# Optimization experiments

Measured on AMD Instinct MI355X. Metric: run time of the kernel, lower is better.

Reference implementation:

```python
import jax, jax.numpy as jnp
import numpy as np

BAND = 8          # band_width
DS = 0.1          # diag_subtract
DILATIONS = (1, 2, 4)
EPS_NORM = 1e-6
EPS_GAP = 1e-6
EPS_LN = 1e-5


def _conv1d(x, w, b, dil=1):
    # x: (B, C_in, T), w: (C_out, C_in, K) torch-style OIH
    pad = dil * (w.shape[-1] // 2)  # 'same' padding as in torch module
    y = jax.lax.conv_general_dilated(
        x, w, window_strides=(1,), padding=[(pad, pad)],
        rhs_dilation=(dil,), dimension_numbers=("NCH", "OIH", "NCH"))
    return y + b[None, :, None]


def _strip(feat, mask, w, ds):
    # Banded cosine SSM: strip[b, idx, t] = ((xn[b,t].xn[b,t+|k|]) - ds*[k==0] + 1)/2 * m[t]*m[t+|k|]
    # Mathematically identical to full S = xn xn^T (symmetric) followed by
    # extract_diagonal_strip, but computes only the (2w+1)-wide band.
    xm = feat * mask[:, :, None]
    xn = xm / (jnp.linalg.norm(xm, axis=-1, keepdims=True) + EPS_NORM)
    T = xn.shape[1]
    rows = []
    for k in range(-w, w + 1):
        a = abs(k)
        dot = jnp.einsum("btd,btd->bt", xn[:, :T - a] if a else xn, xn[:, a:])
        s = (dot - (ds if k == 0 else 0.0) + 1.0) * 0.5
        s = s * mask[:, :T - a] * mask[:, a:] if a else s * mask * mask
        rows.append(jnp.pad(s, ((0, 0), (0, a))))
    return jnp.stack(rows, axis=1)  # (B, 2w+1, T)


def _encode(strip, mask, w_in, b_in, stages):
    h = jax.nn.relu(_conv1d(strip, w_in, b_in))
    for (wd, bd, wp, bp, d) in stages:
        h = jax.nn.relu(_conv1d(h, wd, bd, d))   # dilated k=3 conv (dropout=eval no-op)
        h = jax.nn.relu(_conv1d(h, wp, bp))      # pointwise k=1 conv
    m = mask[:, None, :]
    return (h * m).sum(-1) / (m.sum(-1) + EPS_GAP)  # masked GAP -> (B, C)


def setup_inputs() -> dict:
    key = jax.random.key(0)
    ks = jax.random.split(key, 32)
    B, T, D, C, NB = 32, 4096, 256, 64, 2 * BAND + 1
    s = 0.02
    n = lambda k, shp: (jax.random.normal(k, shp, jnp.float32) * s)
    inp = {
        "video_feat": jax.random.normal(ks[0], (B, T, D), jnp.float32),
        "audio_feat": jax.random.normal(ks[1], (B, T, D), jnp.float32),
        "video_mask": jnp.ones((B, T), jnp.float32),
        "audio_mask": jnp.ones((B, T), jnp.float32),
        "w_in": n(ks[2], (C, NB, 1)), "b_in": jnp.zeros((C,), jnp.float32),
        "w_d1": n(ks[3], (C, C, 3)), "b_d1": jnp.zeros((C,), jnp.float32),
        "w_p1": n(ks[4], (C, C, 1)), "b_p1": jnp.zeros((C,), jnp.float32),
        "w_d2": n(ks[5], (C, C, 3)), "b_d2": jnp.zeros((C,), jnp.float32),
        "w_p2": n(ks[6], (C, C, 1)), "b_p2": jnp.zeros((C,), jnp.float32),
        "w_d3": n(ks[7], (C, C, 3)), "b_d3": jnp.zeros((C,), jnp.float32),
        "w_p3": n(ks[8], (C, C, 1)), "b_p3": jnp.zeros((C,), jnp.float32),
        "ln_g": jnp.ones((2 * C,), jnp.float32), "ln_b": jnp.zeros((2 * C,), jnp.float32),
        "mha_w1": n(ks[9], (2 * C, C)), "mha_b1": jnp.zeros((C,), jnp.float32),
        "mha_w2": n(ks[10], (C, 1)), "mha_b2": -jnp.ones((1,), jnp.float32),
        "ffn_w1": n(ks[11], (2 * C, C)), "ffn_b1": jnp.zeros((C,), jnp.float32),
        "ffn_w2": n(ks[12], (C, 1)), "ffn_b2": jnp.zeros((1,), jnp.float32),
    }
    return inp


def reference(video_feat, audio_feat, video_mask, audio_mask,
              w_in, b_in, w_d1, b_d1, w_p1, b_p1, w_d2, b_d2, w_p2, b_p2,
              w_d3, b_d3, w_p3, b_p3, ln_g, ln_b,
              mha_w1, mha_b1, mha_w2, mha_b2, ffn_w1, ffn_b1, ffn_w2, ffn_b2):
    stages = [(w_d1, b_d1, w_p1, b_p1, DILATIONS[0]),
              (w_d2, b_d2, w_p2, b_p2, DILATIONS[1]),
              (w_d3, b_d3, w_p3, b_p3, DILATIONS[2])]
    z_a = _encode(_strip(audio_feat, audio_mask, BAND, DS), audio_mask, w_in, b_in, stages)
    z_v = _encode(_strip(video_feat, video_mask, BAND, DS), video_mask, w_in, b_in, stages)
    f = jnp.concatenate([z_a, z_v], axis=-1)  # (B, 2C), audio first as in torch
    mu = f.mean(-1, keepdims=True)
    var = ((f - mu) ** 2).mean(-1, keepdims=True)
    fn = (f - mu) / jnp.sqrt(var + EPS_LN) * ln_g + ln_b
    g_mha = jax.nn.sigmoid(jax.nn.relu(fn @ mha_w1 + mha_b1) @ mha_w2 + mha_b2)
    g_ffn = jnp.tanh(jax.nn.relu(fn @ ffn_w1 + ffn_b1) @ ffn_w2 + ffn_b2)
    return (g_mha[:, :, None], g_ffn[:, :, None])  # (B,1,1) each
```

## Files before the change

kernel.cpp:

```cpp
#include <hip/hip_runtime.h>
#include <math.h>

#define B_ 32
#define T_ 4096
#define D_ 256
#define C_ 64
#define EPSN 1e-6f
#define EPSG 1e-6f
#define EPSL 1e-5f
#define DS_ 0.1f

typedef short bfrag __attribute__((ext_vector_type(8)));
typedef float f32x4 __attribute__((ext_vector_type(4)));
typedef unsigned short ushort4_t __attribute__((ext_vector_type(4)));
typedef unsigned short ushort8_t __attribute__((ext_vector_type(8)));

static __device__ __forceinline__ unsigned short f2bf(float f) {
    unsigned int u = __builtin_bit_cast(unsigned int, f);
    unsigned int r = u + 0x7fffu + ((u >> 16) & 1u);
    return (unsigned short)(r >> 16);
}
static __device__ __forceinline__ float bf2f(unsigned short u) {
    return __builtin_bit_cast(float, ((unsigned int)u) << 16);
}

static __device__ __forceinline__ f32x4 mfma_bf16(bfrag a, bfrag b, f32x4 c) {
    return __builtin_amdgcn_mfma_f32_16x16x32_bf16(a, b, c, 0, 0, 0);
}

static __device__ __forceinline__ bfrag cvt8(float4 lo, float4 hi) {
    bfrag v;
    v[0] = (short)f2bf(lo.x); v[1] = (short)f2bf(lo.y);
    v[2] = (short)f2bf(lo.z); v[3] = (short)f2bf(lo.w);
    v[4] = (short)f2bf(hi.x); v[5] = (short)f2bf(hi.y);
    v[6] = (short)f2bf(hi.z); v[7] = (short)f2bf(hi.w);
    return v;
}

static __device__ __forceinline__ unsigned int cvtpk(float a, float b) {
    unsigned int r;
    asm("v_cvt_pk_bf16_f32 %0, %1, %2" : "=v"(r) : "v"(a), "v"(b));
    return r;
}

#define GLD16(dst, base, OFF) \
    asm volatile("global_load_dwordx4 %0, %1, off offset:" #OFF \
                 : "=v"(dst) : "v"(base))

__global__ __launch_bounds__(256) void prepack_kernel(
    const float* __restrict__ w_in,
    const float* __restrict__ wd0, const float* __restrict__ wp0,
    const float* __restrict__ wd1, const float* __restrict__ wp1,
    const float* __restrict__ wd2, const float* __restrict__ wp2,
    unsigned short* __restrict__ wk)
{
    int idx = blockIdx.x * 256 + threadIdx.x;
    if (idx >= 1024 + 3 * 16384) return;
    if (idx < 1024) {
        int c = idx >> 4, a = idx & 15;
        float wv = 0.f;
        if (a <= 8) {
            wv = w_in[c * 17 + 8 + a];
            if (a > 0) wv += w_in[c * 17 + 8 - a];
        }
        wk[idx] = f2bf(wv);
    } else {
        int i2 = idx - 1024;
        int s = i2 >> 14;
        int r = i2 & 16383;
        const float* wd = s == 0 ? wd0 : (s == 1 ? wd1 : wd2);
        const float* wp = s == 0 ? wp0 : (s == 1 ? wp1 : wp2);
        unsigned short v;
        if (r < 12288) {
            int c = r / 192, k = r - c * 192;
            int tap = k >> 6, ci = k & 63;
            v = f2bf(wd[c * 192 + ci * 3 + tap]);
        } else {
            v = f2bf(wp[r - 12288]);
        }
        wk[idx] = v;
    }
}

#define NT24 43
#define DTP 18

__global__ __launch_bounds__(256, 2) void strip_kernel(
    const float* __restrict__ feat0, const float* __restrict__ mask0,
    const float* __restrict__ feat1, const float* __restrict__ mask1,
    unsigned short* __restrict__ s16g)
{
    __shared__ float dotbuf[4 * 3 * 16 * DTP];
    __shared__ float scl[104];
    __shared__ float msk[104];

    int bid0 = blockIdx.x;
    int bid  = (bid0 & 7) * 344 + (bid0 >> 3);
    int tile = bid % NT24;
    int rem  = bid / NT24;
    int b    = rem & 31;
    int mod  = rem >> 5;
    int mb   = mod * B_ + b;
    const float* feat = mod ? feat1 : feat0;
    const float* mask = mod ? mask1 : mask0;
    int t0 = tile * 96;
    int tid = threadIdx.x;
    int w = tid >> 6, lane = tid & 63;
    int l15 = lane & 15, lg = lane >> 4;

    if (tid < 104) {
        int tg = t0 + tid;
        msk[tid] = (tg < T_) ? mask[(size_t)b * T_ + tg] : 0.f;
    }

    const float* fb = feat + (size_t)b * T_ * D_;

    {
        int i0 = t0 + 24 * w;
        int tA = i0 + l15;      if (tA >= T_) tA = 0;
        int tB = i0 + 16 + l15; if (tB >= T_) tB = 0;
        const float* pA = fb + (size_t)tA * D_ + lg * 8;
        const float* pB = fb + (size_t)tB * D_ + lg * 8;

        float4 fa[16], fbx[16];
        GLD16(fa[0],  pA, 0);    GLD16(fbx[0],  pB, 0);
        GLD16(fa[1],  pA, 16);   GLD16(fbx[1],  pB, 16);
        GLD16(fa[2],  pA, 128);  GLD16(fbx[2],  pB, 128);
        GLD16(fa[3],  pA, 144);  GLD16(fbx[3],  pB, 144);
        GLD16(fa[4],  pA, 256);  GLD16(fbx[4],  pB, 256);
        GLD16(fa[5],  pA, 272);  GLD16(fbx[5],  pB, 272);
        GLD16(fa[6],  pA, 384);  GLD16(fbx[6],  pB, 384);
        GLD16(fa[7],  pA, 400);  GLD16(fbx[7],  pB, 400);
        GLD16(fa[8],  pA, 512);  GLD16(fbx[8],  pB, 512);
        GLD16(fa[9],  pA, 528);  GLD16(fbx[9],  pB, 528);
        GLD16(fa[10], pA, 640);  GLD16(fbx[10], pB, 640);
        GLD16(fa[11], pA, 656);  GLD16(fbx[11], pB, 656);
        GLD16(fa[12], pA, 768);  GLD16(fbx[12], pB, 768);
        GLD16(fa[13], pA, 784);  GLD16(fbx[13], pB, 784);
        GLD16(fa[14], pA, 896);  GLD16(fbx[14], pB, 896);
        GLD16(fa[15], pA, 912);  GLD16(fbx[15], pB, 912);

        __builtin_amdgcn_sched_barrier(0);
        asm volatile("s_waitcnt vmcnt(0)" ::: "memory");
        __builtin_amdgcn_sched_barrier(0);

        f32x4 a00 = {0.f, 0.f, 0.f, 0.f};
        f32x4 a01 = {0.f, 0.f, 0.f, 0.f};
        f32x4 a11 = {0.f, 0.f, 0.f, 0.f};
        #pragma unroll
        for (int ks = 0; ks < 8; ++ks) {
            bfrag av = cvt8(fa[2 * ks], fa[2 * ks + 1]);
            bfrag bv = cvt8(fbx[2 * ks], fbx[2 * ks + 1]);
            a00 = mfma_bf16(av, av, a00);
            a01 = mfma_bf16(av, bv, a01);
            a11 = mfma_bf16(bv, bv, a11);
        }

        float* base = dotbuf + w * (3 * 16 * DTP);
        #pragma unroll
        for (int r = 0; r < 4; ++r) {
            int row = lg * 4 + r;
            base[row * DTP + l15] = a00[r];
            base[16 * DTP + row * DTP + l15] = a01[r];
            base[32 * DTP + row * DTP + l15] = a11[r];
        }
    }
    __syncthreads();

    if (tid < 104) {
        int ww = tid / 24; if (ww > 3) ww = 3;
        int v = tid - 24 * ww;
        const float* bb = dotbuf + ww * (3 * 16 * DTP);
        float sd = (v < 16) ? bb[v * DTP + v] : bb[32 * DTP + (v - 16) * DTP + (v - 16)];
        float m = msk[tid];
        scl[tid] = m / (m * sqrtf(sd) + EPSN);
    }
    __syncthreads();

    if (tid < 96) {
        int t = t0 + tid;
        if (t < T_) {
            int ww = tid / 24, r = tid - 24 * ww;
            const float* bb = dotbuf + ww * (3 * 16 * DTP);
            float m_t = msk[tid], sc_t = scl[tid];
            ushort8_t o0, o1;
            #pragma unroll
            for (int e = 0; e < 8; ++e) { o0[e] = 0; o1[e] = 0; }
            #pragma unroll
            for (int a = 0; a <= 8; ++a) {
                int c = r + a;
                float dot;
                if (r < 8)       dot = bb[r * DTP + c];
                else if (r < 16) dot = (c < 16) ? bb[r * DTP + c]
                                               : bb[16 * DTP + r * DTP + (c - 16)];
                else             dot = bb[32 * DTP + (r - 16) * DTP + (c - 16)];
                float dn = dot * sc_t * scl[tid + a];
                float s = (dn - (a == 0 ? DS_ : 0.f) + 1.f) * 0.5f * m_t * msk[tid + a];
                if (a < 8) o0[a] = f2bf(s); else o1[0] = f2bf(s);
            }
            unsigned short* dst = s16g + ((size_t)mb * T_ + t) * 16;
            *(ushort8_t*)dst = o0;
            *(ushort8_t*)(dst + 8) = o1;
        }
    }
}

#define TT 128
#define G_ 16
#define WB 160
#define OFF_BUFA 1024
#define OFF_BUFB 21504
#define SMEM_TOT (41984 + 512)

static __device__ __forceinline__ int swzi(int row, int su, int off) {
    return row * 64 + ((su ^ (row & 7)) << 3) + off;
}

static __device__ __forceinline__ void emit4(unsigned short* dst, f32x4 acc, bool valid) {
    float v0 = valid ? fmaxf(acc[0], 0.f) : 0.f;
    float v1 = valid ? fmaxf(acc[1], 0.f) : 0.f;
    float v2 = valid ? fmaxf(acc[2], 0.f) : 0.f;
    float v3 = valid ? fmaxf(acc[3], 0.f) : 0.f;
    uint2 p;
    p.x = cvtpk(v0, v1);
    p.y = cvtpk(v2, v3);
    *(uint2*)dst = p;
}

template<int DIL>
static __device__ __forceinline__ void conv_stage(
    const unsigned short* __restrict__ wdg, const unsigned short* __restrict__ wpg,
    unsigned short* __restrict__ bufIn, unsigned short* __restrict__ bufOut,
    const float* __restrict__ b_d, const float* __restrict__ b_p,
    int t0, int l15, int lg, int mt0, int wn)
{
    {
        bfrag ad[2][6];
        f32x4 bd[2];
        #pragma unroll
        for (int m = 0; m < 2; ++m) {
            int row = (mt0 + m) * 16 + l15;
            #pragma unroll
            for (int ks = 0; ks < 6; ++ks) {
                int tap = ks >> 1, half = ks & 1;
                ad[m][ks] = *(const bfrag*)(wdg + row * 192 + tap * 64 + half * 32 + lg * 8);
            }
            #pragma unroll
            for (int r = 0; r < 4; ++r) bd[m][r] = b_d[(mt0 + m) * 16 + lg * 4 + r];
        }
        for (int nt = wn * 5; nt < wn * 5 + 5; ++nt) {
            int j = nt * 16 + l15;
            f32x4 acc0 = bd[0], acc1 = bd[1];
            #pragma unroll
            for (int ks = 0; ks < 6; ++ks) {
                int tap = ks >> 1, half = ks & 1;
                int brow = j + (tap - 1) * DIL;
                bfrag bv = *(const bfrag*)(bufIn + swzi(brow, half * 4 + lg, 0));
                acc0 = mfma_bf16(ad[0][ks], bv, acc0);
                acc1 = mfma_bf16(ad[1][ks], bv, acc1);
            }
            int tg = t0 - G_ + j;
            bool valid = (tg >= 0 && tg < T_);
            emit4(bufOut + swzi(j, (mt0 + 0) * 2 + (lg >> 1), (lg & 1) * 4), acc0, valid);
            emit4(bufOut + swzi(j, (mt0 + 1) * 2 + (lg >> 1), (lg & 1) * 4), acc1, valid);
        }
    }
    __syncthreads();

    {
        bfrag ap[2][2];
        f32x4 bp[2];
        #pragma unroll
        for (int m = 0; m < 2; ++m) {
            int row = (mt0 + m) * 16 + l15;
            #pragma unroll
            for (int half = 0; half < 2; ++half)
                ap[m][half] = *(const bfrag*)(wpg + row * 64 + half * 32 + lg * 8);
            #pragma unroll
            for (int r = 0; r < 4; ++r) bp[m][r] = b_p[(mt0 + m) * 16 + lg * 4 + r];
        }
        for (int nt = wn * 5; nt < wn * 5 + 5; ++nt) {
            int j = nt * 16 + l15;
            f32x4 acc0 = bp[0], acc1 = bp[1];
            #pragma unroll
            for (int half = 0; half < 2; ++half) {
                bfrag bv = *(const bfrag*)(bufOut + swzi(j, half * 4 + lg, 0));
                acc0 = mfma_bf16(ap[0][half], bv, acc0);
                acc1 = mfma_bf16(ap[1][half], bv, acc1);
            }
            int tg = t0 - G_ + j;
            bool valid = (tg >= 0 && tg < T_);
            emit4(bufIn + swzi(j, (mt0 + 0) * 2 + (lg >> 1), (lg & 1) * 4), acc0, valid);
            emit4(bufIn + swzi(j, (mt0 + 1) * 2 + (lg >> 1), (lg & 1) * 4), acc1, valid);
        }
    }
    __syncthreads();
}

__global__ __launch_bounds__(256, 3) void conv_mfma_kernel(
    const unsigned short* __restrict__ s16g,
    const float* __restrict__ mask0, const float* __restrict__ mask1,
    const unsigned short* __restrict__ wk,
    const float* __restrict__ b_in,
    const float* __restrict__ b_d1, const float* __restrict__ b_p1,
    const float* __restrict__ b_d2, const float* __restrict__ b_p2,
    const float* __restrict__ b_d3, const float* __restrict__ b_p3,
    float* __restrict__ z_part)
{
    __shared__ __align__(16) char smem[SMEM_TOT];
    float* red = (float*)smem;
    unsigned short* bufA = (unsigned short*)(smem + OFF_BUFA);
    unsigned short* bufB = (unsigned short*)(smem + OFF_BUFB);

    int bid  = blockIdx.x;
    int tile = bid & 31;
    int b    = (bid >> 5) & 31;
    int mod  = bid >> 10;
    int mb   = mod * B_ + b;
    const float* mask = mod ? mask1 : mask0;
    int t0  = tile * TT;
    int tid = threadIdx.x;
    int lane = tid & 63;
    int w = tid >> 6;
    int l15 = lane & 15, lg = lane >> 4;
    int wm = w >> 1, wn = w & 1;
    int mt0 = wm * 2;

    {
        const unsigned short* srow = s16g + (size_t)mb * T_ * 16;
        int lg2 = lg & 1;
        bfrag a_in[2];
        f32x4 bi[2];
        #pragma unroll
        for (int m = 0; m < 2; ++m) {
            int row = (mt0 + m) * 16 + l15;
            a_in[m] = *(const bfrag*)(wk + row * 16 + lg2 * 8);
            #pragma unroll
            for (int r = 0; r < 4; ++r) bi[m][r] = b_in[(mt0 + m) * 16 + lg * 4 + r];
        }
        for (int nt = wn * 5; nt < wn * 5 + 5; ++nt) {
            int j = nt * 16 + l15;
            int tg = t0 - G_ + j;
            bool valid = (tg >= 0 && tg < T_);
            bfrag bv = {0, 0, 0, 0, 0, 0, 0, 0};
            if (lg < 2 && valid) bv = *(const bfrag*)(srow + (size_t)tg * 16 + lg * 8);
            f32x4 acc0 = bi[0], acc1 = bi[1];
            acc0 = mfma_bf16(a_in[0], bv, acc0);
            acc1 = mfma_bf16(a_in[1], bv, acc1);
            emit4(bufA + swzi(j, (mt0 + 0) * 2 + (lg >> 1), (lg & 1) * 4), acc0, valid);
            emit4(bufA + swzi(j, (mt0 + 1) * 2 + (lg >> 1), (lg & 1) * 4), acc1, valid);
        }
    }
    __syncthreads();

    conv_stage<1>(wk + 1024,             wk + 1024 + 12288,             bufA, bufB, b_d1, b_p1, t0, l15, lg, mt0, wn);
    conv_stage<2>(wk + 1024 + 16384,     wk + 1024 + 16384 + 12288,     bufA, bufB, b_d2, b_p2, t0, l15, lg, mt0, wn);
    conv_stage<4>(wk + 1024 + 2 * 16384, wk + 1024 + 2 * 16384 + 12288, bufA, bufB, b_d3, b_p3, t0, l15, lg, mt0, wn);

    {
        int c = tid & 63, g = tid >> 6;
        const float* mrow = mask + (size_t)b * T_ + t0;
        float acc = 0.f;
        #pragma unroll 4
        for (int i = 0; i < 32; ++i) {
            int jj = g * 32 + i;
            int r = G_ + jj;
            acc += bf2f(bufA[swzi(r, c >> 3, c & 7)]) * mrow[jj];
        }
        red[g * 64 + c] = acc;
    }
    __syncthreads();
    if (tid < 64) {
        float z = red[tid] + red[64 + tid] + red[128 + tid] + red[192 + tid];
        z_part[((size_t)mb * 32 + tile) * 64 + tid] = z;
    }
}

__global__ __launch_bounds__(128) void gates_kernel(
    const float* __restrict__ z_part,
    const float* __restrict__ mask0, const float* __restrict__ mask1,
    const float* __restrict__ ln_g, const float* __restrict__ ln_b,
    const float* __restrict__ mha_w1, const float* __restrict__ mha_b1,
    const float* __restrict__ mha_w2, const float* __restrict__ mha_b2,
    const float* __restrict__ ffn_w1, const float* __restrict__ ffn_b1,
    const float* __restrict__ ffn_w2, const float* __restrict__ ffn_b2,
    float* __restrict__ out)
{
    __shared__ float fn[128];
    __shared__ float red[4];
    __shared__ float msum[2];
    int b = blockIdx.x, tid = threadIdx.x;
    int mod = tid >> 6, c = tid & 63;

    float z = 0.f;
    for (int tl = 0; tl < 32; ++tl)
        z += z_part[((size_t)(mod * B_ + b) * 32 + tl) * 64 + c];

    const float* mk = mod ? mask1 : mask0;
    float ms = 0.f;
    for (int t = c; t < T_; t += 64) ms += mk[(size_t)b * T_ + t];
    #pragma unroll
    for (int o = 32; o > 0; o >>= 1) ms += __shfl_xor(ms, o);
    if (c == 0) msum[mod] = ms;
    __syncthreads();

    float fv = z / (msum[mod] + EPSG);
    float s1 = fv, s2 = fv * fv;
    #pragma unroll
    for (int o = 32; o > 0; o >>= 1) { s1 += __shfl_xor(s1, o); s2 += __shfl_xor(s2, o); }
    if (c == 0) { red[mod * 2] = s1; red[mod * 2 + 1] = s2; }
    __syncthreads();

    float mu  = (red[0] + red[2]) * (1.0f / 128.0f);
    float ex2 = (red[1] + red[3]) * (1.0f / 128.0f);
    float var = ex2 - mu * mu;
    float fnv = (fv - mu) * rsqrtf(var + EPSL) * ln_g[tid] + ln_b[tid];
    fn[tid] = fnv;
    __syncthreads();

    const float* W1 = mod ? ffn_w1 : mha_w1;
    const float* B1 = mod ? ffn_b1 : mha_b1;
    const float* W2 = mod ? ffn_w2 : mha_w2;
    const float* B2 = mod ? ffn_b2 : mha_b2;
    float r = B1[c];
    for (int i = 0; i < 128; ++i) r += fn[i] * W1[i * 64 + c];
    r = fmaxf(r, 0.f);
    float g = r * W2[c];
    #pragma unroll
    for (int o = 32; o > 0; o >>= 1) g += __shfl_xor(g, o);
    if (c == 0) {
        g += B2[0];
        out[mod * B_ + b] = mod ? tanhf(g) : 1.0f / (1.0f + expf(-g));
    }
}

extern "C" void kernel_launch(void* const* d_in, const int* in_sizes, int n_in,
                              void* d_out, int out_size, void* d_ws, size_t ws_size,
                              hipStream_t stream) {
    const float* video_feat = (const float*)d_in[0];
    const float* audio_feat = (const float*)d_in[1];
    const float* video_mask = (const float*)d_in[2];
    const float* audio_mask = (const float*)d_in[3];
    const float* w_in = (const float*)d_in[4];
    const float* b_in = (const float*)d_in[5];
    const float* w_d1 = (const float*)d_in[6];
    const float* b_d1 = (const float*)d_in[7];
    const float* w_p1 = (const float*)d_in[8];
    const float* b_p1 = (const float*)d_in[9];
    const float* w_d2 = (const float*)d_in[10];
    const float* b_d2 = (const float*)d_in[11];
    const float* w_p2 = (const float*)d_in[12];
    const float* b_p2 = (const float*)d_in[13];
    const float* w_d3 = (const float*)d_in[14];
    const float* b_d3 = (const float*)d_in[15];
    const float* w_p3 = (const float*)d_in[16];
    const float* b_p3 = (const float*)d_in[17];
    const float* ln_g = (const float*)d_in[18];
    const float* ln_b = (const float*)d_in[19];
    const float* mha_w1 = (const float*)d_in[20];
    const float* mha_b1 = (const float*)d_in[21];
    const float* mha_w2 = (const float*)d_in[22];
    const float* mha_b2 = (const float*)d_in[23];
    const float* ffn_w1 = (const float*)d_in[24];
    const float* ffn_b1 = (const float*)d_in[25];
    const float* ffn_w2 = (const float*)d_in[26];
    const float* ffn_b2 = (const float*)d_in[27];

    unsigned short* s16g = (unsigned short*)d_ws;
    float* z_part = (float*)((char*)d_ws + (size_t)2 * B_ * T_ * 16 * 2);
    unsigned short* wk = (unsigned short*)((char*)z_part + (size_t)2 * B_ * 32 * 64 * 4);

    prepack_kernel<<<dim3(196), dim3(256), 0, stream>>>(
        w_in, w_d1, w_p1, w_d2, w_p2, w_d3, w_p3, wk);

    strip_kernel<<<dim3(2 * B_ * NT24), dim3(256), 0, stream>>>(
        audio_feat, audio_mask, video_feat, video_mask, s16g);

    conv_mfma_kernel<<<dim3(2 * B_ * (T_ / TT)), dim3(256), 0, stream>>>(
        s16g, audio_mask, video_mask, wk, b_in,
        b_d1, b_p1, b_d2, b_p2, b_d3, b_p3, z_part);

    gates_kernel<<<dim3(B_), dim3(128), 0, stream>>>(
        z_part, audio_mask, video_mask, ln_g, ln_b,
        mha_w1, mha_b1, mha_w2, mha_b2, ffn_w1, ffn_b1, ffn_w2, ffn_b2,
        (float*)d_out);
}
```

Baseline: 138.2 us.

## Software-pipeline strip kernel over two tile groups per block with split loads

Each strip block now handles two consecutive 96-row tile groups of a sequence instead of one. Feature loads are split into two halves so the next group's loads are issued while the current group's MFMAs run. The per-wave normalisation and output stage is made wave-local to drop two block-wide barriers. The grid halves, so there are fewer blocks to hide latency, and the number of registers held live grows.

```diff
diff --git a/kernel.cpp b/kernel.cpp
--- a/kernel.cpp
+++ b/kernel.cpp
@@ -82,127 +82,158 @@
     }
 }
 
-#define NT24 43
-#define DTP 18
+#define SEQB 22
+#define TPB 2
 
 __global__ __launch_bounds__(256, 2) void strip_kernel(
     const float* __restrict__ feat0, const float* __restrict__ mask0,
     const float* __restrict__ feat1, const float* __restrict__ mask1,
     unsigned short* __restrict__ s16g)
 {
-    __shared__ float dotbuf[4 * 3 * 16 * DTP];
-    __shared__ float scl[104];
-    __shared__ float msk[104];
+    __shared__ float dotbuf[4 * 864];
+    __shared__ float sclw[4 * 32];
+    __shared__ float mskb[208];
 
     int bid0 = blockIdx.x;
-    int bid  = (bid0 & 7) * 344 + (bid0 >> 3);
-    int tile = bid % NT24;
-    int rem  = bid / NT24;
-    int b    = rem & 31;
-    int mod  = rem >> 5;
+    int bid  = (bid0 & 7) * 176 + (bid0 >> 3);
+    int seq  = bid / SEQB;
+    int blk  = bid - seq * SEQB;
+    int b    = seq & 31;
+    int mod  = seq >> 5;
     int mb   = mod * B_ + b;
     const float* feat = mod ? feat1 : feat0;
     const float* mask = mod ? mask1 : mask0;
-    int t0 = tile * 96;
+    int first = blk * TPB;
+    int ngr   = (43 - first < TPB) ? (43 - first) : TPB;
+    int base0 = first * 96;
     int tid = threadIdx.x;
     int w = tid >> 6, lane = tid & 63;
     int l15 = lane & 15, lg = lane >> 4;
 
-    if (tid < 104) {
-        int tg = t0 + tid;
-        msk[tid] = (tg < T_) ? mask[(size_t)b * T_ + tg] : 0.f;
-    }
+    if (tid < 208) {
+        int tg = base0 + tid;
+        mskb[tid] = (tg < T_) ? mask[(size_t)b * T_ + tg] : 0.f;
+    }
+    __syncthreads();
 
     const float* fb = feat + (size_t)b * T_ * D_;
 
-    {
-        int i0 = t0 + 24 * w;
+    float4 fa0[8], fb0[8], fa1[8], fb1[8];
+    const float *pA, *pB;
+
+    auto setaddr = [&](int g) {
+        int i0 = (first + g) * 96 + 24 * w;
         int tA = i0 + l15;      if (tA >= T_) tA = 0;
         int tB = i0 + 16 + l15; if (tB >= T_) tB = 0;
-        const float* pA = fb + (size_t)tA * D_ + lg * 8;
-        const float* pB = fb + (size_t)tB * D_ + lg * 8;
-
-        float4 fa[16], fbx[16];
-        GLD16(fa[0],  pA, 0);    GLD16(fbx[0],  pB, 0);
-        GLD16(fa[1],  pA, 16);   GLD16(fbx[1],  pB, 16);
-        GLD16(fa[2],  pA, 128);  GLD16(fbx[2],  pB, 128);
-        GLD16(fa[3],  pA, 144);  GLD16(fbx[3],  pB, 144);
-        GLD16(fa[4],  pA, 256);  GLD16(fbx[4],  pB, 256);
-        GLD16(fa[5],  pA, 272);  GLD16(fbx[5],  pB, 272);
-        GLD16(fa[6],  pA, 384);  GLD16(fbx[6],  pB, 384);
-        GLD16(fa[7],  pA, 400);  GLD16(fbx[7],  pB, 400);
-        GLD16(fa[8],  pA, 512);  GLD16(fbx[8],  pB, 512);
-        GLD16(fa[9],  pA, 528);  GLD16(fbx[9],  pB, 528);
-        GLD16(fa[10], pA, 640);  GLD16(fbx[10], pB, 640);
-        GLD16(fa[11], pA, 656);  GLD16(fbx[11], pB, 656);
-        GLD16(fa[12], pA, 768);  GLD16(fbx[12], pB, 768);
-        GLD16(fa[13], pA, 784);  GLD16(fbx[13], pB, 784);
-        GLD16(fa[14], pA, 896);  GLD16(fbx[14], pB, 896);
-        GLD16(fa[15], pA, 912);  GLD16(fbx[15], pB, 912);
+        pA = fb + (size_t)tA * D_ + lg * 8;
+        pB = fb + (size_t)tB * D_ + lg * 8;
+    };
+
+#define ISSUE_C0() do { \
+    GLD16(fa0[0], pA, 0);   GLD16(fb0[0], pB, 0);   \
+    GLD16(fa0[1], pA, 16);  GLD16(fb0[1], pB, 16);  \
+    GLD16(fa0[2], pA, 128); GLD16(fb0[2], pB, 128); \
+    GLD16(fa0[3], pA, 144); GLD16(fb0[3], pB, 144); \
+    GLD16(fa0[4], pA, 256); GLD16(fb0[4], pB, 256); \
+    GLD16(fa0[5], pA, 272); GLD16(fb0[5], pB, 272); \
+    GLD16(fa0[6], pA, 384); GLD16(fb0[6], pB, 384); \
+    GLD16(fa0[7], pA, 400); GLD16(fb0[7], pB, 400); } while (0)
+
+#define ISSUE_C1() do { \
+    GLD16(fa1[0], pA, 512); GLD16(fb1[0], pB, 512); \
+    GLD16(fa1[1], pA, 528); GLD16(fb1[1], pB, 528); \
+    GLD16(fa1[2], pA, 640); GLD16(fb1[2], pB, 640); \
+    GLD16(fa1[3], pA, 656); GLD16(fb1[3], pB, 656); \
+    GLD16(fa1[4], pA, 768); GLD16(fb1[4], pB, 768); \
+    GLD16(fa1[5], pA, 784); GLD16(fb1[5], pB, 784); \
+    GLD16(fa1[6], pA, 896); GLD16(fb1[6], pB, 896); \
+    GLD16(fa1[7], pA, 912); GLD16(fb1[7], pB, 912); } while (0)
+
+    setaddr(0);
+    ISSUE_C0();
+    ISSUE_C1();
+
+    for (int g = 0; g < ngr; ++g) {
+        bool nxt = (g + 1 < ngr);
 
         __builtin_amdgcn_sched_barrier(0);
-        asm volatile("s_waitcnt vmcnt(0)" ::: "memory");
+        asm volatile("s_waitcnt vmcnt(16)" ::: "memory");
         __builtin_amdgcn_sched_barrier(0);
 
         f32x4 a00 = {0.f, 0.f, 0.f, 0.f};
         f32x4 a01 = {0.f, 0.f, 0.f, 0.f};
         f32x4 a11 = {0.f, 0.f, 0.f, 0.f};
         #pragma unroll
-        for (int ks = 0; ks < 8; ++ks) {
-            bfrag av = cvt8(fa[2 * ks], fa[2 * ks + 1]);
-            bfrag bv = cvt8(fbx[2 * ks], fbx[2 * ks + 1]);
+        for (int ks = 0; ks < 4; ++ks) {
+            bfrag av = cvt8(fa0[2 * ks], fa0[2 * ks + 1]);
+            bfrag bv = cvt8(fb0[2 * ks], fb0[2 * ks + 1]);
             a00 = mfma_bf16(av, av, a00);
             a01 = mfma_bf16(av, bv, a01);
             a11 = mfma_bf16(bv, bv, a11);
         }
 
-        float* base = dotbuf + w * (3 * 16 * DTP);
+        if (nxt) { setaddr(g + 1); ISSUE_C0(); }
+
+        __builtin_amdgcn_sched_barrier(0);
+        if (nxt) asm volatile("s_waitcnt vmcnt(16)" ::: "memory");
+        else     asm volatile("s_waitcnt vmcnt(0)"  ::: "memory");
+        __builtin_amdgcn_sched_barrier(0);
+
+        #pragma unroll
+        for (int ks = 0; ks < 4; ++ks) {
+            bfrag av = cvt8(fa1[2 * ks], fa1[2 * ks + 1]);
+            bfrag bv = cvt8(fb1[2 * ks], fb1[2 * ks + 1]);
+            a00 = mfma_bf16(av, av, a00);
+            a01 = mfma_bf16(av, bv, a01);
+            a11 = mfma_bf16(bv, bv, a11);
+        }
+
+        if (nxt) ISSUE_C1();
+
+        int i0 = (first + g) * 96 + 24 * w;
+        float* bb = dotbuf + w * 864;
         #pragma unroll
         for (int r = 0; r < 4; ++r) {
             int row = lg * 4 + r;
-            base[row * DTP + l15] = a00[r];
-            base[16 * DTP + row * DTP + l15] = a01[r];
-            base[32 * DTP + row * DTP + l15] = a11[r];
-        }
-    }
-    __syncthreads();
-
-    if (tid < 104) {
-        int ww = tid / 24; if (ww > 3) ww = 3;
-        int v = tid - 24 * ww;
-        const float* bb = dotbuf + ww * (3 * 16 * DTP);
-        float sd = (v < 16) ? bb[v * DTP + v] : bb[32 * DTP + (v - 16) * DTP + (v - 16)];
-        float m = msk[tid];
-        scl[tid] = m / (m * sqrtf(sd) + EPSN);
-    }
-    __syncthreads();
-
-    if (tid < 96) {
-        int t = t0 + tid;
-        if (t < T_) {
-            int ww = tid / 24, r = tid - 24 * ww;
-            const float* bb = dotbuf + ww * (3 * 16 * DTP);
-            float m_t = msk[tid], sc_t = scl[tid];
-            ushort8_t o0, o1;
-            #pragma unroll
-            for (int e = 0; e < 8; ++e) { o0[e] = 0; o1[e] = 0; }
-            #pragma unroll
-            for (int a = 0; a <= 8; ++a) {
-                int c = r + a;
-                float dot;
-                if (r < 8)       dot = bb[r * DTP + c];
-                else if (r < 16) dot = (c < 16) ? bb[r * DTP + c]
-                                               : bb[16 * DTP + r * DTP + (c - 16)];
-                else             dot = bb[32 * DTP + (r - 16) * DTP + (c - 16)];
-                float dn = dot * sc_t * scl[tid + a];
-                float s = (dn - (a == 0 ? DS_ : 0.f) + 1.f) * 0.5f * m_t * msk[tid + a];
-                if (a < 8) o0[a] = f2bf(s); else o1[0] = f2bf(s);
+            bb[row * 18 + l15] = a00[r];
+            bb[288 + row * 18 + l15] = a01[r];
+            bb[576 + row * 18 + l15] = a11[r];
+        }
+        if (lane < 32) {
+            int v = lane;
+            float sd = (v < 16) ? bb[v * 18 + v] : bb[576 + (v - 16) * 18 + (v - 16)];
+            float m = mskb[i0 - base0 + v];
+            sclw[w * 32 + v] = m / (m * sqrtf(sd) + EPSN);
+        }
+        if (lane < 24) {
+            int r = lane;
+            int tglob = i0 + r;
+            if (tglob < T_) {
+                int rel = i0 - base0 + r;
+                float m_t = mskb[rel], sc_t = sclw[w * 32 + r];
+                ushort8_t o0, o1;
+                #pragma unroll
+                for (int e = 0; e < 8; ++e) { o0[e] = 0; o1[e] = 0; }
+                #pragma unroll
+                for (int a = 0; a <= 8; ++a) {
+                    int c = r + a;
+                    float dot;
+                    if (r < 8)       dot = bb[r * 18 + c];
+                    else if (r < 16) dot = (c < 16) ? bb[r * 18 + c]
+                                                   : bb[288 + r * 18 + (c - 16)];
+                    else             dot = bb[576 + (r - 16) * 18 + (c - 16)];
+                    float dn = dot * sc_t * sclw[w * 32 + r + a];
+                    float s = (dn - (a == 0 ? DS_ : 0.f) + 1.f) * 0.5f * m_t * mskb[rel + a];
+                    if (a < 8) o0[a] = f2bf(s); else o1[0] = f2bf(s);
+                }
+                unsigned short* dst = s16g + ((size_t)mb * T_ + tglob) * 16;
+                *(ushort8_t*)dst = o0;
+                *(ushort8_t*)(dst + 8) = o1;
             }
-            unsigned short* dst = s16g + ((size_t)mb * T_ + t) * 16;
-            *(ushort8_t*)dst = o0;
-            *(ushort8_t*)(dst + 8) = o1;
-        }
-    }
+        }
+    }
+#undef ISSUE_C0
+#undef ISSUE_C1
 }
 
 #define TT 128
@@ -473,7 +504,7 @@
     prepack_kernel<<<dim3(196), dim3(256), 0, stream>>>(
         w_in, w_d1, w_p1, w_d2, w_p2, w_d3, w_p3, wk);
 
-    strip_kernel<<<dim3(2 * B_ * NT24), dim3(256), 0, stream>>>(
+    strip_kernel<<<dim3(64 * SEQB), dim3(256), 0, stream>>>(
         audio_feat, audio_mask, video_feat, video_mask, s16g);
 
     conv_mfma_kernel<<<dim3(2 * B_ * (T_ / TT)), dim3(256), 0, stream>>>(
```

After: 144.7 us. +4.7%, slower.
